# Kernel tuning notes

Hardware: AMD Instinct MI355X
Metric: run time of the kernel (lower is better)

Reference implementation:

```python
import jax, jax.numpy as jnp
import numpy as np
import math

B, N, D, H, F, L, T, V = 2, 1024, 256, 8, 1024, 2, 2, 32000
DH = D // H
ALPHA = 0.1  # phase_alpha


def _ln(x, g, b):
    m = jnp.mean(x, -1, keepdims=True)
    v = jnp.mean((x - m) ** 2, -1, keepdims=True)
    return (x - m) * jax.lax.rsqrt(v + 1e-5) * g + b


def setup_inputs() -> dict:
    key = jax.random.key(0)
    ks = iter(jax.random.split(key, 40))
    def nrm(shape, s):
        return jax.random.normal(next(ks), shape, jnp.float32) * s
    s = 1.0 / math.sqrt(D)
    inp = {}
    inp['input_ids'] = jax.random.randint(next(ks), (B, N), 0, V)
    inp['tok_emb'] = nrm((V, D), 0.02)
    inp['pos_emb'] = nrm((N, D), 0.02)
    inp['en_g'] = jnp.ones((D,)); inp['en_b'] = jnp.zeros((D,))
    inp['pi_w'] = nrm((D, H), s); inp['pi_b'] = jnp.zeros((H,))
    inp['Wq'] = nrm((L, D, D), s); inp['Wk'] = nrm((L, D, D), s)
    inp['Wv'] = nrm((L, D, D), s); inp['Wo'] = nrm((L, D, D), s)
    inp['pp_w'] = nrm((L, D, H), s); inp['pp_b'] = jnp.zeros((L, H))
    inp['f1_w'] = nrm((L, D, F), s); inp['f1_b'] = jnp.zeros((L, F))
    inp['f2_w'] = nrm((L, F, D), 1.0 / math.sqrt(F)); inp['f2_b'] = jnp.zeros((L, D))
    inp['ln1_g'] = jnp.ones((L, D)); inp['ln1_b'] = jnp.zeros((L, D))
    inp['ln2_g'] = jnp.ones((L, D)); inp['ln2_b'] = jnp.zeros((L, D))
    inp['pu_w'] = nrm((L, D, H), s); inp['pu_b'] = jnp.zeros((L, H))
    inp['on_g'] = jnp.ones((D,)); inp['on_b'] = jnp.zeros((D,))
    inp['head_w'] = nrm((D, V), s); inp['head_b'] = jnp.zeros((V,))
    return inp


def reference(input_ids, tok_emb, pos_emb, en_g, en_b, pi_w, pi_b,
              Wq, Wk, Wv, Wo, pp_w, pp_b, f1_w, f1_b, f2_w, f2_b,
              ln1_g, ln1_b, ln2_g, ln2_b, pu_w, pu_b, on_g, on_b,
              head_w, head_b):
    # Embedding + positional + LayerNorm (dropout=0 / eval mode)
    h = tok_emb[input_ids] + pos_emb[None, :, :]          # (B,N,D)
    h = _ln(h, en_g, en_b)
    phases = h @ pi_w + pi_b                              # (B,N,H) threaded state
    scale = 1.0 / math.sqrt(DH)
    # Iterated shared-structure blocks (early stop never fires with random init)
    for t in range(T):
        for l in range(L):
            # --- HarmonicEdgeLayer ---
            q = (h @ Wq[l]).reshape(B, N, H, DH)
            k = (h @ Wk[l]).reshape(B, N, H, DH)
            scores = jnp.einsum('bihk,bjhk->bhij', q, k) * scale   # (B,H,N,N)
            ph = (h @ pp_w[l] + pp_b[l]).transpose(0, 2, 1)         # (B,H,N)
            mod = jnp.cos(ph[:, :, :, None] - ph[:, :, None, :])    # (B,H,N,N)
            scores = scores * (1.0 + mod) * 0.5
            ew = jax.nn.softmax(scores, axis=-1)
            # --- HarmonicNodeUpdate ---
            v = (h @ Wv[l]).reshape(B, N, H, DH)
            msg = jnp.einsum('bhij,bjhk->bihk', ew, v).reshape(B, N, D) @ Wo[l]
            h = _ln(h + msg, ln1_g[l], ln1_b[l])
            ff = jax.nn.gelu(h @ f1_w[l] + f1_b[l], approximate=False) @ f2_w[l] + f2_b[l]
            h = _ln(h + ff, ln2_g[l], ln2_b[l])
            # --- PhaseUpdate (state carried; does not feed edge weights) ---
            phases = phases + ALPHA * jnp.tanh(h @ pu_w[l] + pu_b[l]) * math.pi
    h = _ln(h, on_g, on_b)
    pooled = h.mean(axis=1)                               # mean readout, no mask
    return pooled @ head_w + head_b                       # (B, V)
```

## Files before the change

kernel.cpp:

```cpp
#include <hip/hip_runtime.h>
#include <hip/hip_bf16.h>
#include <math.h>

#define DV 256
#define NSEQ 1024
#define HHEADS 8
#define VV 32000
#define QKSCALE 0.17677669529663687f

typedef __attribute__((ext_vector_type(8))) short short8v;
typedef __attribute__((ext_vector_type(4))) float f32x4;

__device__ __forceinline__ unsigned short f2bf(float f){
  __hip_bfloat16 b = __float2bfloat16(f);
  return *reinterpret_cast<unsigned short*>(&b);
}
__device__ __forceinline__ float bfbits2f(unsigned short u){
  unsigned int x = ((unsigned int)u) << 16;
  return __uint_as_float(x);
}

#define OFF_WQKVP 0
#define OFF_WOT   425984
#define OFF_F1T   557056
#define OFF_F2T   1081344
__global__ __launch_bounds__(256) void transpose_cvt_all(
    const float* __restrict__ Wq, const float* __restrict__ Wk,
    const float* __restrict__ Wv, const float* __restrict__ Wo,
    const float* __restrict__ ppw, const float* __restrict__ f1w,
    const float* __restrict__ f2w, __hip_bfloat16* __restrict__ dst){
  __shared__ float sh[32][33];
  int bid = blockIdx.x;
  int t = threadIdx.x;
  if(bid >= 512 && bid < 528){
    int idx = bid - 512;
    int l = idx >> 3, k0 = (idx & 7) * 32;
    int rowo = t >> 2;
    int kbase = k0 + (t & 3) * 8;
    unsigned short vals[8];
    if(rowo < 8){
      int hh = rowo;
      #pragma unroll
      for(int i=0;i<8;i++) vals[i] = f2bf(ppw[(long)l*2048 + (kbase+i)*HHEADS + hh]);
    } else {
      #pragma unroll
      for(int i=0;i<8;i++) vals[i] = 0;
    }
    unsigned short* d = (unsigned short*)dst + (long)l*212992 + (768+rowo)*256 + kbase;
    #pragma unroll
    for(int i=0;i<8;i++) d[i] = vals[i];
    return;
  }
  const float* src; __hip_bfloat16* d; int K, N, tile;
  if(bid < 384){
    int l = bid / 192, rem = bid % 192, mat = rem >> 6; tile = rem & 63;
    src = (mat==0 ? Wq : (mat==1 ? Wk : Wv)) + l*65536;
    d = dst + (long)l*212992 + mat*65536;
    K = 256; N = 256;
  } else if(bid < 512){
    int b2 = bid - 384; int l = b2 >> 6; tile = b2 & 63;
    src = Wo + l*65536; d = dst + OFF_WOT + l*65536; K = 256; N = 256;
  } else if(bid < 1040){
    int b2 = bid - 528; int l = b2 >> 8; tile = b2 & 255;
    src = f1w + l*262144; d = dst + OFF_F1T + l*262144; K = 256; N = 1024;
  } else {
    int b2 = bid - 1040; int l = b2 >> 8; tile = b2 & 255;
    src = f2w + l*262144; d = dst + OFF_F2T + l*262144; K = 1024; N = 256;
  }
  int ntn = N >> 5;
  int tk = tile / ntn, tn = tile - tk*ntn;
  int k0 = tk*32, n0 = tn*32;
  {
    int rr = t >> 3, cc = (t & 7) * 4;
    float4 v = *(const float4*)&src[(long)(k0+rr)*N + n0 + cc];
    sh[rr][cc]=v.x; sh[rr][cc+1]=v.y; sh[rr][cc+2]=v.z; sh[rr][cc+3]=v.w;
  }
  __syncthreads();
  int nn = t >> 3, kk = (t & 7) * 4;
  ushort4 o;
  o.x = f2bf(sh[kk+0][nn]);
  o.y = f2bf(sh[kk+1][nn]);
  o.z = f2bf(sh[kk+2][nn]);
  o.w = f2bf(sh[kk+3][nn]);
  *(ushort4*)&((unsigned short*)d)[(long)(n0+nn)*K + k0 + kk] = o;
}

__global__ __launch_bounds__(256) void embed_ln_kernel(
    const int* __restrict__ ids, const float* __restrict__ tok, const float* __restrict__ pos,
    const float* __restrict__ g, const float* __restrict__ bt,
    float* __restrict__ h, __hip_bfloat16* __restrict__ hb){
  int t = threadIdx.x;
  int lane = t & 63;
  int row = blockIdx.x*4 + (t >> 6);
  int n = row & (NSEQ-1);
  int id = ids[row];
  float4 vv = ((const float4*)tok)[(long)id*64 + lane];
  float4 pv = ((const float4*)pos)[n*64 + lane];
  vv.x += pv.x; vv.y += pv.y; vv.z += pv.z; vv.w += pv.w;
  float s  = vv.x+vv.y+vv.z+vv.w;
  float s2 = vv.x*vv.x+vv.y*vv.y+vv.z*vv.z+vv.w*vv.w;
  #pragma unroll
  for(int off=1; off<64; off<<=1){ s += __shfl_xor(s, off); s2 += __shfl_xor(s2, off); }
  float mean = s*(1.f/DV);
  float var = fmaxf(s2*(1.f/DV) - mean*mean, 0.f);
  float inv = rsqrtf(var + 1e-5f);
  float4 gv = ((const float4*)g)[lane];
  float4 bv = ((const float4*)bt)[lane];
  float4 o;
  o.x=(vv.x-mean)*inv*gv.x+bv.x; o.y=(vv.y-mean)*inv*gv.y+bv.y;
  o.z=(vv.z-mean)*inv*gv.z+bv.z; o.w=(vv.w-mean)*inv*gv.w+bv.w;
  ((float4*)h)[row*64 + lane] = o;
  ushort4 ob; ob.x=f2bf(o.x); ob.y=f2bf(o.y); ob.z=f2bf(o.z); ob.w=f2bf(o.w);
  *(ushort4*)&hb[row*DV + lane*4] = ob;
}

__global__ __launch_bounds__(256) void ln_res_kernel(
    const float* __restrict__ x, const float* __restrict__ r,
    float* __restrict__ out, __hip_bfloat16* __restrict__ outb,
    const float* __restrict__ g, const float* __restrict__ bt){
  int t = threadIdx.x;
  int lane = t & 63;
  int row = blockIdx.x*4 + (t >> 6);
  float4 vv = ((const float4*)x)[row*64 + lane];
  float4 rv = ((const float4*)r)[row*64 + lane];
  vv.x += rv.x; vv.y += rv.y; vv.z += rv.z; vv.w += rv.w;
  float s  = vv.x+vv.y+vv.z+vv.w;
  float s2 = vv.x*vv.x+vv.y*vv.y+vv.z*vv.z+vv.w*vv.w;
  #pragma unroll
  for(int off=1; off<64; off<<=1){ s += __shfl_xor(s, off); s2 += __shfl_xor(s2, off); }
  float mean = s*(1.f/DV);
  float var = fmaxf(s2*(1.f/DV) - mean*mean, 0.f);
  float inv = rsqrtf(var + 1e-5f);
  float4 gv = ((const float4*)g)[lane];
  float4 bv = ((const float4*)bt)[lane];
  float4 o;
  o.x=(vv.x-mean)*inv*gv.x+bv.x; o.y=(vv.y-mean)*inv*gv.y+bv.y;
  o.z=(vv.z-mean)*inv*gv.z+bv.z; o.w=(vv.w-mean)*inv*gv.w+bv.w;
  ((float4*)out)[row*64 + lane] = o;
  ushort4 ob; ob.x=f2bf(o.x); ob.y=f2bf(o.y); ob.z=f2bf(o.z); ob.w=f2bf(o.w);
  *(ushort4*)&outb[row*DV + lane*4] = ob;
}

template<int WM, int WN, int FM, int FN, int ACT, int OUT_BF16, int PHASE>
__global__ __launch_bounds__(256) void mfma_gemm(
    const __hip_bfloat16* __restrict__ A, const __hip_bfloat16* __restrict__ Bt,
    const float* __restrict__ bias, void* __restrict__ Cout,
    int M, int N, int K, int ldc,
    const float* __restrict__ pb, float* __restrict__ cph, float* __restrict__ sph){
  constexpr int BM = WM*FM*16;
  constexpr int BN = WN*FN*16;
  constexpr int TPRA = 256/BM;
  constexpr int JA = 16/TPRA;
  __shared__ short As[2][BM][136];
  __shared__ short Bs[2][BN][136];
  int tm = blockIdx.x*BM, tn = blockIdx.y*BN;
  int t = threadIdx.x;
  int lane = t & 63, w = t >> 6;
  int wm = w / WN, wn = w % WN;
  int lr = lane & 15, lg = lane >> 4;
  f32x4 acc[FM][FN] = {};
  const short* gA = (const short*)A;
  const short* gB = (const short*)Bt;
  int ra = t / TPRA, ca = t % TPRA;
  int rb = t >> 2,  cb = t & 3;
  short8v ar[JA], br[4];
#define LOADC(K0) { const short* pa = &gA[(long)(tm+ra)*K + (K0)]; \
    _Pragma("unroll") for(int j=0;j<JA;j++) ar[j] = *(const short8v*)&pa[(ca+TPRA*j)*8]; \
    const short* pbp = &gB[(long)(tn+rb)*K + (K0)]; \
    _Pragma("unroll") for(int j=0;j<4;j++) br[j] = *(const short8v*)&pbp[(cb+4*j)*8]; }
#define STOREC(BUF) { _Pragma("unroll") for(int j=0;j<JA;j++) *(short8v*)&As[BUF][ra][(ca+TPRA*j)*8] = ar[j]; \
    _Pragma("unroll") for(int j=0;j<4;j++) *(short8v*)&Bs[BUF][rb][(cb+4*j)*8] = br[j]; }
  int nch = K >> 7;
  LOADC(0);
  STOREC(0);
  if(nch > 1) LOADC(128);
  __syncthreads();
  for(int c=0; c<nch; c++){
    int cur = c & 1;
    #pragma unroll
    for(int ks=0; ks<4; ks++){
      short8v af[FM], bf[FN];
      #pragma unroll
      for(int i=0;i<FM;i++) af[i] = *(const short8v*)&As[cur][wm*FM*16 + i*16 + lr][ks*32 + lg*8];
      #pragma unroll
      for(int j=0;j<FN;j++) bf[j] = *(const short8v*)&Bs[cur][wn*FN*16 + j*16 + lr][ks*32 + lg*8];
      #pragma unroll
      for(int i=0;i<FM;i++)
        #pragma unroll
        for(int j=0;j<FN;j++)
          acc[i][j] = __builtin_amdgcn_mfma_f32_16x16x32_bf16(af[i], bf[j], acc[i][j], 0,0,0);
    }
    if(c+1 < nch){
      STOREC(cur^1);
      if(c+2 < nch) LOADC((c+2)*128);
    }
    __syncthreads();
  }
#undef LOADC
#undef STOREC
  if(PHASE && tn >= N - 64){
    #pragma unroll
    for(int fn=0; fn<FN; fn++){
      int colr = wn*FN*16 + fn*16 + lr;
      if(colr < 8){
        float bb = pb[colr];
        #pragma unroll
        for(int fm=0; fm<FM; fm++){
          int row0 = tm + wm*FM*16 + fm*16 + lg*4;
          #pragma unroll
          for(int r2=0; r2<4; r2++){
            float ph = acc[fm][fn][r2] + bb;
            float sv, cv;
            __sincosf(ph, &sv, &cv);
            int row = row0 + r2;
            int b = row >> 10, n = row & 1023;
            int idx = (b*HHEADS + colr)*NSEQ + n;
            cph[idx] = cv; sph[idx] = sv;
          }
        }
      }
    }
    return;
  }
  #pragma unroll
  for(int fn=0; fn<FN; fn++){
    int col = tn + wn*FN*16 + fn*16 + lr;
    float bs = bias ? bias[col] : 0.f;
    #pragma unroll
    for(int fm=0; fm<FM; fm++){
      int row0 = tm + wm*FM*16 + fm*16 + lg*4;
      #pragma unroll
      for(int r2=0; r2<4; r2++){
        float xx = acc[fm][fn][r2] + bs;
        if(ACT == 1) xx = 0.5f*xx*(1.f + erff(xx*0.70710678118654752f));
        long idx = (long)(row0+r2)*ldc + col;
        if(OUT_BF16) ((__hip_bfloat16*)Cout)[idx] = __float2bfloat16(xx);
        else         ((float*)Cout)[idx] = xx;
      }
    }
  }
}

__global__ __launch_bounds__(256) void attn_mfma_kernel(
    const __hip_bfloat16* __restrict__ qkv,
    const float* __restrict__ cph, const float* __restrict__ sph,
    __hip_bfloat16* __restrict__ po, float* __restrict__ ml){
  __shared__ __align__(16) short K2[2][64][104];
  __shared__ __align__(16) short V2[2][32][72];
  __shared__ __align__(16) short Pp[4][16][72];
  int bid = blockIdx.x;
  int bh = bid >> 6;
  int qt = (bid >> 2) & 15;
  int ks = bid & 3;
  int b = bh >> 3, hh = bh & 7;
  int t = threadIdx.x;
  int lane = t & 63, w = t >> 6;
  int lr = lane & 15, lg = lane >> 4;
  int q0w = qt*64 + w*16;

  const unsigned short* qrow = (const unsigned short*)qkv
      + ((long)(b*NSEQ + q0w + lr))*768 + hh*32 + lg*8;
  short8v qraw = *(const short8v*)qrow;
  float ci = cph[bh*NSEQ + q0w + lr];
  float si = sph[bh*NSEQ + q0w + lr];
  short8v qf0, qf1, qf2;
  #pragma unroll
  for(int i=0;i<8;i++){
    float x = bfbits2f((unsigned short)qraw[i]) * (0.5f*QKSCALE);
    qf0[i] = (short)f2bf(x);
    qf1[i] = (short)f2bf(x*ci);
    qf2[i] = (short)f2bf(x*si);
  }

  int srow = t >> 2, sdc = (t & 3) * 8;
  int j0b = ks*4;
  short8v kv, vvr; float cj, sj;
#define LOADT(J) { long rg = (long)(b*NSEQ + (J)*64 + srow)*768; \
    kv  = *(const short8v*)((const unsigned short*)qkv + rg + 256 + hh*32 + sdc); \
    vvr = *(const short8v*)((const unsigned short*)qkv + rg + 512 + hh*32 + sdc); \
    cj = cph[bh*NSEQ + (J)*64 + srow]; sj = sph[bh*NSEQ + (J)*64 + srow]; }
#define STORET(BUF) { short8v kc, ksv; \
    _Pragma("unroll") for(int i=0;i<8;i++){ float x = bfbits2f((unsigned short)kv[i]); \
      kc[i] = (short)f2bf(x*cj); ksv[i] = (short)f2bf(x*sj); } \
    *(short8v*)&K2[BUF][srow][sdc]    = kv; \
    *(short8v*)&K2[BUF][srow][32+sdc] = kc; \
    *(short8v*)&K2[BUF][srow][64+sdc] = ksv; \
    _Pragma("unroll") for(int i=0;i<8;i++) V2[BUF][sdc+i][srow] = vvr[i]; }

  float l = 0.f;
  f32x4 acc[2] = {};

  LOADT(j0b);
  STORET(0);
  LOADT(j0b+1);
  __syncthreads();
  for(int j=0; j<4; j++){
    int cur = j & 1;
    f32x4 st[4];
    #pragma unroll
    for(int kt=0; kt<4; kt++){
      short8v a0 = *(const short8v*)&K2[cur][kt*16+lr][lg*8];
      short8v a1 = *(const short8v*)&K2[cur][kt*16+lr][32+lg*8];
      short8v a2 = *(const short8v*)&K2[cur][kt*16+lr][64+lg*8];
      f32x4 z = {0.f,0.f,0.f,0.f};
      z = __builtin_amdgcn_mfma_f32_16x16x32_bf16(a0, qf0, z, 0,0,0);
      z = __builtin_amdgcn_mfma_f32_16x16x32_bf16(a1, qf1, z, 0,0,0);
      z = __builtin_amdgcn_mfma_f32_16x16x32_bf16(a2, qf2, z, 0,0,0);
      st[kt] = z;
    }
    float ls = 0.f;
    #pragma unroll
    for(int kt=0; kt<4; kt++){
      float p0 = __expf(st[kt][0]);
      float p1 = __expf(st[kt][1]);
      float p2 = __expf(st[kt][2]);
      float p3 = __expf(st[kt][3]);
      ls += (p0+p1)+(p2+p3);
      unsigned int w0 = (unsigned)f2bf(p0) | ((unsigned)f2bf(p1)<<16);
      unsigned int w1 = (unsigned)f2bf(p2) | ((unsigned)f2bf(p3)<<16);
      unsigned int* pp = (unsigned int*)&Pp[w][lr][kt*16 + lg*4];
      pp[0] = w0; pp[1] = w1;
    }
    ls += __shfl_xor(ls, 16);
    ls += __shfl_xor(ls, 32);
    l += ls;
    #pragma unroll
    for(int kk=0; kk<2; kk++){
      short8v pa  = *(const short8v*)&Pp[w][lr][kk*32 + lg*8];
      short8v vf0 = *(const short8v*)&V2[cur][lr][kk*32 + lg*8];
      short8v vf1 = *(const short8v*)&V2[cur][16+lr][kk*32 + lg*8];
      acc[0] = __builtin_amdgcn_mfma_f32_16x16x32_bf16(pa, vf0, acc[0], 0,0,0);
      acc[1] = __builtin_amdgcn_mfma_f32_16x16x32_bf16(pa, vf1, acc[1], 0,0,0);
    }
    if(j < 3){
      STORET(cur^1);
      if(j < 2) LOADT(j0b+j+2);
    }
    __syncthreads();
  }
#undef LOADT
#undef STORET
  if(lane < 16){
    ml[((long)(ks*16+bh))*NSEQ + q0w + lr] = l;
  }
  #pragma unroll
  for(int dt=0; dt<2; dt++)
    #pragma unroll
    for(int r=0;r<4;r++){
      int row = q0w + lg*4 + r;
      po[(((long)(ks*16+bh))*NSEQ + row)*32 + dt*16 + lr] =
          __float2bfloat16(acc[dt][r]);
    }
}

__global__ __launch_bounds__(256) void wo_ln_kernel(
    const __hip_bfloat16* __restrict__ po, const float* __restrict__ ml,
    const __hip_bfloat16* __restrict__ Bt, const float* __restrict__ hres,
    const float* __restrict__ lng, const float* __restrict__ lnb,
    float* __restrict__ h1, __hip_bfloat16* __restrict__ hb1){
  __shared__ short As[16][264];
  __shared__ short Bs[64][264];
  __shared__ float Co[16][260];
  int tm = blockIdx.x*16;
  int t = threadIdx.x;
  int lane = t & 63, w = t >> 6;
  int lr = lane & 15, lg = lane >> 4;
  {
    int r = t >> 4;
    int c16 = (t & 15) * 16;
    int R = tm + r; int b = R >> 10, q = R & 1023;
    int bh = b*HHEADS + (c16 >> 5);
    long mlb = (long)bh*NSEQ + q;
    float lsum = ml[mlb] + ml[mlb + 16*NSEQ] + ml[mlb + 32*NSEQ] + ml[mlb + 48*NSEQ];
    float inv = 1.f/lsum;
    long pob = ((long)bh*NSEQ + q)*32 + (c16 & 31);
    const unsigned short* pp = (const unsigned short*)po;
    #pragma unroll
    for(int i=0;i<2;i++){
      short8v a0 = *(const short8v*)&pp[pob + i*8];
      short8v a1 = *(const short8v*)&pp[pob + (long)16*NSEQ*32 + i*8];
      short8v a2 = *(const short8v*)&pp[pob + (long)32*NSEQ*32 + i*8];
      short8v a3 = *(const short8v*)&pp[pob + (long)48*NSEQ*32 + i*8];
      short8v o;
      #pragma unroll
      for(int k=0;k<8;k++)
        o[k] = (short)f2bf((bfbits2f((unsigned short)a0[k]) + bfbits2f((unsigned short)a1[k])
                          + bfbits2f((unsigned short)a2[k]) + bfbits2f((unsigned short)a3[k]))*inv);
      *(short8v*)&As[r][c16 + i*8] = o;
    }
  }
  const short* gB = (const short*)Bt;
  int rb = t >> 2, cb = t & 3;
  {
    const short* pbp = &gB[(long)rb*256];
    #pragma unroll
    for(int j=0;j<8;j++) *(short8v*)&Bs[rb][(cb+4*j)*8] = *(const short8v*)&pbp[(cb+4*j)*8];
  }
  __syncthreads();
  f32x4 acc[4] = {};
  for(int ct=0; ct<4; ct++){
    #pragma unroll
    for(int ksx=0; ksx<8; ksx++){
      short8v af = *(const short8v*)&As[lr][ksx*32 + lg*8];
      short8v bf = *(const short8v*)&Bs[w*16+lr][ksx*32 + lg*8];
      acc[ct] = __builtin_amdgcn_mfma_f32_16x16x32_bf16(af, bf, acc[ct], 0,0,0);
    }
    if(ct < 3){
      __syncthreads();
      const short* pbp = &gB[(long)((ct+1)*64 + rb)*256];
      #pragma unroll
      for(int j=0;j<8;j++) *(short8v*)&Bs[rb][(cb+4*j)*8] = *(const short8v*)&pbp[(cb+4*j)*8];
      __syncthreads();
    }
  }
  #pragma unroll
  for(int ct=0; ct<4; ct++)
    #pragma unroll
    for(int r2=0; r2<4; r2++)
      Co[lg*4 + r2][ct*64 + w*16 + lr] = acc[ct][r2];
  __syncthreads();
  {
    int r = t >> 4;
    int c16 = (t & 15) * 16;
    int R = tm + r;
    float v[16];
    float s = 0.f, s2 = 0.f;
    const float* hr = hres + (long)R*DV + c16;
    #pragma unroll
    for(int i=0;i<4;i++){
      float4 hv = *(const float4*)&hr[4*i];
      float x0 = Co[r][c16+4*i]   + hv.x;
      float x1 = Co[r][c16+4*i+1] + hv.y;
      float x2 = Co[r][c16+4*i+2] + hv.z;
      float x3 = Co[r][c16+4*i+3] + hv.w;
      v[4*i]=x0; v[4*i+1]=x1; v[4*i+2]=x2; v[4*i+3]=x3;
      s += x0+x1+x2+x3;
      s2 += x0*x0+x1*x1+x2*x2+x3*x3;
    }
    s += __shfl_xor(s,1); s2 += __shfl_xor(s2,1);
    s += __shfl_xor(s,2); s2 += __shfl_xor(s2,2);
    s += __shfl_xor(s,4); s2 += __shfl_xor(s2,4);
    s += __shfl_xor(s,8); s2 += __shfl_xor(s2,8);
    float mean = s*(1.f/DV);
    float var = fmaxf(s2*(1.f/DV) - mean*mean, 0.f);
    float invs = rsqrtf(var + 1e-5f);
    #pragma unroll
    for(int i=0;i<4;i++){
      int col = c16 + 4*i;
      float4 gv = *(const float4*)&lng[col];
      float4 bv = *(const float4*)&lnb[col];
      float o0 = (v[4*i+0]-mean)*invs*gv.x + bv.x;
      float o1 = (v[4*i+1]-mean)*invs*gv.y + bv.y;
      float o2 = (v[4*i+2]-mean)*invs*gv.z + bv.z;
      float o3 = (v[4*i+3]-mean)*invs*gv.w + bv.w;
      *(float4*)&h1[(long)R*DV + col] = make_float4(o0,o1,o2,o3);
      ushort4 ob; ob.x=f2bf(o0); ob.y=f2bf(o1); ob.z=f2bf(o2); ob.w=f2bf(o3);
      *(ushort4*)&hb1[(long)R*DV + col] = ob;
    }
  }
}

__global__ __launch_bounds__(256) void final_pool_kernel(
    const float* __restrict__ x, const float* __restrict__ r,
    const float* __restrict__ g2, const float* __restrict__ b2,
    const float* __restrict__ og, const float* __restrict__ ob,
    float* __restrict__ part){
  __shared__ float ws2[32][260];
  int t = threadIdx.x;
  int lrow = t >> 3;
  int row = blockIdx.x*32 + lrow;
  int c0 = (t & 7) * 32;
  float v[32];
  float s=0.f, s2=0.f;
  const float* xr = x + (long)row*DV + c0;
  const float* rr = r + (long)row*DV + c0;
  #pragma unroll
  for(int i=0;i<8;i++){
    float4 xv = *(const float4*)&xr[4*i];
    float4 rv = *(const float4*)&rr[4*i];
    xv.x+=rv.x; xv.y+=rv.y; xv.z+=rv.z; xv.w+=rv.w;
    v[4*i]=xv.x; v[4*i+1]=xv.y; v[4*i+2]=xv.z; v[4*i+3]=xv.w;
    s += xv.x+xv.y+xv.z+xv.w;
    s2 += xv.x*xv.x+xv.y*xv.y+xv.z*xv.z+xv.w*xv.w;
  }
  s += __shfl_xor(s,1); s2 += __shfl_xor(s2,1);
  s += __shfl_xor(s,2); s2 += __shfl_xor(s2,2);
  s += __shfl_xor(s,4); s2 += __shfl_xor(s2,4);
  float mean = s*(1.f/DV);
  float var = fmaxf(s2*(1.f/DV)-mean*mean, 0.f);
  float inv = rsqrtf(var + 1e-5f);
  float s_=0.f, s2_=0.f;
  #pragma unroll
  for(int i=0;i<32;i++){
    int col = c0 + i;
    float o = (v[i]-mean)*inv*g2[col] + b2[col];
    v[i] = o;
    s_ += o; s2_ += o*o;
  }
  s_ += __shfl_xor(s_,1); s2_ += __shfl_xor(s2_,1);
  s_ += __shfl_xor(s_,2); s2_ += __shfl_xor(s2_,2);
  s_ += __shfl_xor(s_,4); s2_ += __shfl_xor(s2_,4);
  float mean2 = s_*(1.f/DV);
  float var2 = fmaxf(s2_*(1.f/DV)-mean2*mean2, 0.f);
  float inv2 = rsqrtf(var2 + 1e-5f);
  #pragma unroll
  for(int i=0;i<32;i++){
    int col = c0 + i;
    ws2[lrow][col] = (v[i]-mean2)*inv2*og[col] + ob[col];
  }
  __syncthreads();
  float accv = 0.f;
  #pragma unroll 8
  for(int rr2=0; rr2<32; rr2++) accv += ws2[rr2][t];
  part[blockIdx.x*DV + t] = accv;
}

__global__ __launch_bounds__(256) void head_kernel(
    const float* __restrict__ part, const float* __restrict__ W,
    const float* __restrict__ hb, float* __restrict__ out){
  __shared__ float pooled[2][256];
  int t = threadIdx.x;
  float a0 = 0.f, a1 = 0.f;
  #pragma unroll 8
  for(int k=0;k<32;k++){ a0 += part[k*DV + t]; a1 += part[(32+k)*DV + t]; }
  pooled[0][t] = a0 * (1.f/NSEQ);
  pooled[1][t] = a1 * (1.f/NSEQ);
  __syncthreads();
  int vcol = blockIdx.x*256 + t;
  float x0 = 0.f, x1 = 0.f;
  #pragma unroll 8
  for(int d=0; d<DV; d++){
    float wv = W[(long)d*VV + vcol];
    x0 += pooled[0][d]*wv;
    x1 += pooled[1][d]*wv;
  }
  float bb = hb[vcol];
  out[vcol] = x0 + bb;
  out[VV + vcol] = x1 + bb;
}

extern "C" void kernel_launch(void* const* d_in, const int* in_sizes, int n_in,
                              void* d_out, int out_size, void* d_ws, size_t ws_size,
                              hipStream_t stream){
  const int*   ids   = (const int*)  d_in[0];
  const float* tok   = (const float*)d_in[1];
  const float* pos   = (const float*)d_in[2];
  const float* en_g  = (const float*)d_in[3];
  const float* en_b  = (const float*)d_in[4];
  const float* Wq    = (const float*)d_in[7];
  const float* Wk    = (const float*)d_in[8];
  const float* Wv    = (const float*)d_in[9];
  const float* Wo    = (const float*)d_in[10];
  const float* pp_w  = (const float*)d_in[11];
  const float* pp_b  = (const float*)d_in[12];
  const float* f1_w  = (const float*)d_in[13];
  const float* f1_b  = (const float*)d_in[14];
  const float* f2_w  = (const float*)d_in[15];
  const float* f2_b  = (const float*)d_in[16];
  const float* ln1_g = (const float*)d_in[17];
  const float* ln1_b = (const float*)d_in[18];
  const float* ln2_g = (const float*)d_in[19];
  const float* ln2_b = (const float*)d_in[20];
  const float* on_g  = (const float*)d_in[23];
  const float* on_b  = (const float*)d_in[24];
  const float* head_w= (const float*)d_in[25];
  const float* head_b= (const float*)d_in[26];
  float* out = (float*)d_out;

  char* wsb = (char*)d_ws;
  float* h    = (float*)(wsb);
  __hip_bfloat16* hb  = (__hip_bfloat16*)(wsb + (2u<<20));
  float* h1   = (float*)(wsb + (3u<<20));
  __hip_bfloat16* hb1 = (__hip_bfloat16*)(wsb + (5u<<20));
  __hip_bfloat16* qkv = (__hip_bfloat16*)(wsb + (6u<<20));
  __hip_bfloat16* po  = (__hip_bfloat16*)(wsb + (9u<<20));
  float* mlb  = (float*)(wsb + (13u<<20));
  __hip_bfloat16* ff  = (__hip_bfloat16*)(wsb + (14u<<20));
  float* s_ff = (float*)(wsb + (18u<<20));
  float* cphb = (float*)(wsb + (20u<<20));
  float* sphb = cphb + 16384;
  float* part = sphb + 16384;
  __hip_bfloat16* wt = (__hip_bfloat16*)(wsb + (20u<<20) + (192u<<10));
  __hip_bfloat16* wqkvp = wt + OFF_WQKVP;
  __hip_bfloat16* wot   = wt + OFF_WOT;
  __hip_bfloat16* f1t   = wt + OFF_F1T;
  __hip_bfloat16* f2t   = wt + OFF_F2T;

  transpose_cvt_all<<<1552, 256, 0, stream>>>(Wq, Wk, Wv, Wo, pp_w, f1_w, f2_w, wt);
  embed_ln_kernel<<<512, 256, 0, stream>>>(ids, tok, pos, en_g, en_b, h, hb);

  for(int it=0; it<4; it++){
    int l = it & 1;
    mfma_gemm<2,2,2,2, 0,1,1><<<dim3(32,13), 256, 0, stream>>>(
        hb, wqkvp + (long)l*212992, nullptr, qkv, 2048, 832, 256, 768,
        pp_b + l*HHEADS, cphb, sphb);
    attn_mfma_kernel<<<1024, 256, 0, stream>>>(qkv, cphb, sphb, po, mlb);
    wo_ln_kernel<<<128, 256, 0, stream>>>(
        po, mlb, wot + l*65536, h, ln1_g + l*DV, ln1_b + l*DV, h1, hb1);
    mfma_gemm<2,2,2,2, 1,1,0><<<dim3(32,16), 256, 0, stream>>>(
        hb1, f1t + l*262144, f1_b + l*1024, ff, 2048, 1024, 256, 1024,
        nullptr, nullptr, nullptr);
    mfma_gemm<1,4,2,1, 0,0,0><<<dim3(64,4), 256, 0, stream>>>(
        ff, f2t + l*262144, f2_b + l*DV, s_ff, 2048, 256, 1024, 256,
        nullptr, nullptr, nullptr);
    if(it < 3)
      ln_res_kernel<<<512, 256, 0, stream>>>(s_ff, h1, h, hb, ln2_g + l*DV, ln2_b + l*DV);
  }
  final_pool_kernel<<<64, 256, 0, stream>>>(s_ff, h1, ln2_g + DV, ln2_b + DV, on_g, on_b, part);
  head_kernel<<<125, 256, 0, stream>>>(part, head_w, head_b, out);
}
```

Before: 205.8 us.

## Halve GEMM K-chunk and single-buffer attention LDS with register prefetch

The GEMM kernel's LDS staging chunk drops from 128 to 64 along K, which halves shared memory per block so more blocks can be resident. The attention kernel goes from double-buffered LDS tiles to one buffer, with two register sets used for prefetch and a fully unrolled schedule. The trade is more barriers and more loop iterations, and the attention path needs an extra sync pair per tile in exchange for lower LDS use and possibly higher occupancy.

```diff
diff --git a/kernel.cpp b/kernel.cpp
--- a/kernel.cpp
+++ b/kernel.cpp
@@ -150,9 +150,11 @@
   constexpr int BM = WM*FM*16;
   constexpr int BN = WN*FN*16;
   constexpr int TPRA = 256/BM;
-  constexpr int JA = 16/TPRA;
-  __shared__ short As[2][BM][136];
-  __shared__ short Bs[2][BN][136];
+  constexpr int JA = 8/TPRA;
+  constexpr int TPRB = 256/BN;
+  constexpr int JB = 8/TPRB;
+  __shared__ short As[2][BM][72];
+  __shared__ short Bs[2][BN][72];
   int tm = blockIdx.x*BM, tn = blockIdx.y*BN;
   int t = threadIdx.x;
   int lane = t & 63, w = t >> 6;
@@ -162,23 +164,23 @@
   const short* gA = (const short*)A;
   const short* gB = (const short*)Bt;
   int ra = t / TPRA, ca = t % TPRA;
-  int rb = t >> 2,  cb = t & 3;
-  short8v ar[JA], br[4];
+  int rb = t / TPRB, cb = t % TPRB;
+  short8v ar[JA], br[JB];
 #define LOADC(K0) { const short* pa = &gA[(long)(tm+ra)*K + (K0)]; \
     _Pragma("unroll") for(int j=0;j<JA;j++) ar[j] = *(const short8v*)&pa[(ca+TPRA*j)*8]; \
     const short* pbp = &gB[(long)(tn+rb)*K + (K0)]; \
-    _Pragma("unroll") for(int j=0;j<4;j++) br[j] = *(const short8v*)&pbp[(cb+4*j)*8]; }
+    _Pragma("unroll") for(int j=0;j<JB;j++) br[j] = *(const short8v*)&pbp[(cb+TPRB*j)*8]; }
 #define STOREC(BUF) { _Pragma("unroll") for(int j=0;j<JA;j++) *(short8v*)&As[BUF][ra][(ca+TPRA*j)*8] = ar[j]; \
-    _Pragma("unroll") for(int j=0;j<4;j++) *(short8v*)&Bs[BUF][rb][(cb+4*j)*8] = br[j]; }
-  int nch = K >> 7;
+    _Pragma("unroll") for(int j=0;j<JB;j++) *(short8v*)&Bs[BUF][rb][(cb+TPRB*j)*8] = br[j]; }
+  int nch = K >> 6;
   LOADC(0);
   STOREC(0);
-  if(nch > 1) LOADC(128);
+  LOADC(64);
   __syncthreads();
   for(int c=0; c<nch; c++){
     int cur = c & 1;
     #pragma unroll
-    for(int ks=0; ks<4; ks++){
+    for(int ks=0; ks<2; ks++){
       short8v af[FM], bf[FN];
       #pragma unroll
       for(int i=0;i<FM;i++) af[i] = *(const short8v*)&As[cur][wm*FM*16 + i*16 + lr][ks*32 + lg*8];
@@ -192,7 +194,7 @@
     }
     if(c+1 < nch){
       STOREC(cur^1);
-      if(c+2 < nch) LOADC((c+2)*128);
+      if(c+2 < nch) LOADC((c+2)*64);
     }
     __syncthreads();
   }
@@ -245,8 +247,8 @@
     const __hip_bfloat16* __restrict__ qkv,
     const float* __restrict__ cph, const float* __restrict__ sph,
     __hip_bfloat16* __restrict__ po, float* __restrict__ ml){
-  __shared__ __align__(16) short K2[2][64][104];
-  __shared__ __align__(16) short V2[2][32][72];
+  __shared__ __align__(16) short K2[64][104];
+  __shared__ __align__(16) short V2[32][72];
   __shared__ __align__(16) short Pp[4][16][72];
   int bid = blockIdx.x;
   int bh = bid >> 6;
@@ -274,72 +276,78 @@
 
   int srow = t >> 2, sdc = (t & 3) * 8;
   int j0b = ks*4;
-  short8v kv, vvr; float cj, sj;
-#define LOADT(J) { long rg = (long)(b*NSEQ + (J)*64 + srow)*768; \
-    kv  = *(const short8v*)((const unsigned short*)qkv + rg + 256 + hh*32 + sdc); \
-    vvr = *(const short8v*)((const unsigned short*)qkv + rg + 512 + hh*32 + sdc); \
-    cj = cph[bh*NSEQ + (J)*64 + srow]; sj = sph[bh*NSEQ + (J)*64 + srow]; }
-#define STORET(BUF) { short8v kc, ksv; \
-    _Pragma("unroll") for(int i=0;i<8;i++){ float x = bfbits2f((unsigned short)kv[i]); \
-      kc[i] = (short)f2bf(x*cj); ksv[i] = (short)f2bf(x*sj); } \
-    *(short8v*)&K2[BUF][srow][sdc]    = kv; \
-    *(short8v*)&K2[BUF][srow][32+sdc] = kc; \
-    *(short8v*)&K2[BUF][srow][64+sdc] = ksv; \
-    _Pragma("unroll") for(int i=0;i<8;i++) V2[BUF][sdc+i][srow] = vvr[i]; }
+  short8v kvA, vvA, kvB, vvB; float cjA, sjA, cjB, sjB;
+#define LOADT(KV,VV,CJ,SJ,J) { long rg = (long)(b*NSEQ + (J)*64 + srow)*768; \
+    KV = *(const short8v*)((const unsigned short*)qkv + rg + 256 + hh*32 + sdc); \
+    VV = *(const short8v*)((const unsigned short*)qkv + rg + 512 + hh*32 + sdc); \
+    CJ = cph[bh*NSEQ + (J)*64 + srow]; SJ = sph[bh*NSEQ + (J)*64 + srow]; }
+#define STORET(KV,VV,CJ,SJ) { short8v kc, ksv; \
+    _Pragma("unroll") for(int i=0;i<8;i++){ float x = bfbits2f((unsigned short)KV[i]); \
+      kc[i] = (short)f2bf(x*CJ); ksv[i] = (short)f2bf(x*SJ); } \
+    *(short8v*)&K2[srow][sdc]    = KV; \
+    *(short8v*)&K2[srow][32+sdc] = kc; \
+    *(short8v*)&K2[srow][64+sdc] = ksv; \
+    _Pragma("unroll") for(int i=0;i<8;i++) V2[sdc+i][srow] = VV[i]; }
 
   float l = 0.f;
   f32x4 acc[2] = {};
 
-  LOADT(j0b);
-  STORET(0);
-  LOADT(j0b+1);
-  __syncthreads();
-  for(int j=0; j<4; j++){
-    int cur = j & 1;
-    f32x4 st[4];
-    #pragma unroll
-    for(int kt=0; kt<4; kt++){
-      short8v a0 = *(const short8v*)&K2[cur][kt*16+lr][lg*8];
-      short8v a1 = *(const short8v*)&K2[cur][kt*16+lr][32+lg*8];
-      short8v a2 = *(const short8v*)&K2[cur][kt*16+lr][64+lg*8];
-      f32x4 z = {0.f,0.f,0.f,0.f};
-      z = __builtin_amdgcn_mfma_f32_16x16x32_bf16(a0, qf0, z, 0,0,0);
-      z = __builtin_amdgcn_mfma_f32_16x16x32_bf16(a1, qf1, z, 0,0,0);
-      z = __builtin_amdgcn_mfma_f32_16x16x32_bf16(a2, qf2, z, 0,0,0);
-      st[kt] = z;
-    }
-    float ls = 0.f;
-    #pragma unroll
-    for(int kt=0; kt<4; kt++){
-      float p0 = __expf(st[kt][0]);
-      float p1 = __expf(st[kt][1]);
-      float p2 = __expf(st[kt][2]);
-      float p3 = __expf(st[kt][3]);
-      ls += (p0+p1)+(p2+p3);
-      unsigned int w0 = (unsigned)f2bf(p0) | ((unsigned)f2bf(p1)<<16);
-      unsigned int w1 = (unsigned)f2bf(p2) | ((unsigned)f2bf(p3)<<16);
-      unsigned int* pp = (unsigned int*)&Pp[w][lr][kt*16 + lg*4];
-      pp[0] = w0; pp[1] = w1;
-    }
-    ls += __shfl_xor(ls, 16);
-    ls += __shfl_xor(ls, 32);
-    l += ls;
-    #pragma unroll
-    for(int kk=0; kk<2; kk++){
-      short8v pa  = *(const short8v*)&Pp[w][lr][kk*32 + lg*8];
-      short8v vf0 = *(const short8v*)&V2[cur][lr][kk*32 + lg*8];
-      short8v vf1 = *(const short8v*)&V2[cur][16+lr][kk*32 + lg*8];
-      acc[0] = __builtin_amdgcn_mfma_f32_16x16x32_bf16(pa, vf0, acc[0], 0,0,0);
-      acc[1] = __builtin_amdgcn_mfma_f32_16x16x32_bf16(pa, vf1, acc[1], 0,0,0);
-    }
-    if(j < 3){
-      STORET(cur^1);
-      if(j < 2) LOADT(j0b+j+2);
-    }
-    __syncthreads();
-  }
+#define ROUND(PF) { \
+    f32x4 st[4]; \
+    _Pragma("unroll") for(int kt=0; kt<4; kt++){ \
+      short8v a0 = *(const short8v*)&K2[kt*16+lr][lg*8]; \
+      short8v a1 = *(const short8v*)&K2[kt*16+lr][32+lg*8]; \
+      short8v a2 = *(const short8v*)&K2[kt*16+lr][64+lg*8]; \
+      f32x4 z = {0.f,0.f,0.f,0.f}; \
+      z = __builtin_amdgcn_mfma_f32_16x16x32_bf16(a0, qf0, z, 0,0,0); \
+      z = __builtin_amdgcn_mfma_f32_16x16x32_bf16(a1, qf1, z, 0,0,0); \
+      z = __builtin_amdgcn_mfma_f32_16x16x32_bf16(a2, qf2, z, 0,0,0); \
+      st[kt] = z; \
+    } \
+    PF; \
+    float ls = 0.f; \
+    _Pragma("unroll") for(int kt=0; kt<4; kt++){ \
+      float p0 = __expf(st[kt][0]); \
+      float p1 = __expf(st[kt][1]); \
+      float p2 = __expf(st[kt][2]); \
+      float p3 = __expf(st[kt][3]); \
+      ls += (p0+p1)+(p2+p3); \
+      unsigned int w0 = (unsigned)f2bf(p0) | ((unsigned)f2bf(p1)<<16); \
+      unsigned int w1 = (unsigned)f2bf(p2) | ((unsigned)f2bf(p3)<<16); \
+      unsigned int* pp = (unsigned int*)&Pp[w][lr][kt*16 + lg*4]; \
+      pp[0] = w0; pp[1] = w1; \
+    } \
+    ls += __shfl_xor(ls, 16); \
+    ls += __shfl_xor(ls, 32); \
+    l += ls; \
+    _Pragma("unroll") for(int kk=0; kk<2; kk++){ \
+      short8v pa  = *(const short8v*)&Pp[w][lr][kk*32 + lg*8]; \
+      short8v vf0 = *(const short8v*)&V2[lr][kk*32 + lg*8]; \
+      short8v vf1 = *(const short8v*)&V2[16+lr][kk*32 + lg*8]; \
+      acc[0] = __builtin_amdgcn_mfma_f32_16x16x32_bf16(pa, vf0, acc[0], 0,0,0); \
+      acc[1] = __builtin_amdgcn_mfma_f32_16x16x32_bf16(pa, vf1, acc[1], 0,0,0); \
+    } }
+
+  LOADT(kvA, vvA, cjA, sjA, j0b);
+  STORET(kvA, vvA, cjA, sjA);
+  LOADT(kvB, vvB, cjB, sjB, j0b+1);
+  __syncthreads();
+  ROUND( LOADT(kvA, vvA, cjA, sjA, j0b+2) );
+  __syncthreads();
+  STORET(kvB, vvB, cjB, sjB);
+  __syncthreads();
+  ROUND( LOADT(kvB, vvB, cjB, sjB, j0b+3) );
+  __syncthreads();
+  STORET(kvA, vvA, cjA, sjA);
+  __syncthreads();
+  ROUND(;);
+  __syncthreads();
+  STORET(kvB, vvB, cjB, sjB);
+  __syncthreads();
+  ROUND(;);
 #undef LOADT
 #undef STORET
+#undef ROUND
   if(lane < 16){
     ml[((long)(ks*16+bh))*NSEQ + q0w + lr] = l;
   }
```

After: 213.0 us. +3.5%, slower.
